# Kernel tuning notes

Hardware: AMD Instinct MI355X
Metric: run time of the kernel (lower is better)

## Reference

```python
import jax, jax.numpy as jnp
import numpy as np

B, V = 128, 128000


def setup_inputs() -> dict:
    key = jax.random.key(0)
    k1, k2, k3, k4 = jax.random.split(key, 4)
    logits = jax.random.normal(k1, (B, V), dtype=jnp.float32) * 4.0
    k = jax.random.randint(k2, (B,), 1, 1024, dtype=jnp.int32)  # top-k per row, >= 1
    p = jax.random.uniform(k3, (B,), dtype=jnp.float32, minval=0.5, maxval=1.0)
    # Exponential(1) noise, matching torch q.exponential_() in random_sample
    q = jax.random.exponential(k4, (B, V), dtype=jnp.float32)
    return {"logits": logits, "k": k, "p": p, "q": q}


def _apply_top_k_top_p(logits, k, p):
    # Faithful port of apply_top_k_top_p_pytorch (sort-ascending path).
    b, v = logits.shape
    idx = jnp.argsort(logits, axis=-1)                       # ascending, [B, V]
    ls = jnp.take_along_axis(logits, idx, axis=-1)           # sorted logits
    # top-k: threshold = (v-k)-th smallest sorted logit; values below -> -inf
    kth = jnp.take_along_axis(ls, (v - k.astype(jnp.int32))[:, None], axis=-1)  # [B, 1]
    ls = jnp.where(ls < kth, -jnp.inf, ls)
    # top-p: mask smallest tail whose cumulative prob <= 1 - p (never mask last col)
    probs_sort = jax.nn.softmax(ls, axis=-1)
    csum = jnp.cumsum(probs_sort, axis=-1)
    top_p_mask = csum <= (1.0 - p)[:, None]
    top_p_mask = top_p_mask.at[:, -1].set(False)
    ls = jnp.where(top_p_mask, -jnp.inf, ls)
    # scatter back to original vocab order
    rows = jnp.arange(b)[:, None]
    return jnp.zeros_like(logits).at[rows, idx].set(ls)


def reference(logits, k, p, q):
    # forward_native with logprobs_mode='raw_logprobs' (returns sampled ids)
    masked = _apply_top_k_top_p(logits, k, p)
    probs = jax.nn.softmax(masked, axis=-1)                  # fp32 softmax
    # Gumbel-max / exponential-race sampling: argmax(probs / Exp(1))
    token_ids = jnp.argmax(probs / q, axis=-1)
    return token_ids
```

## Files before the change

### kernel.cpp

```cpp
#include <hip/hip_runtime.h>
#include <stdint.h>

#define V 128000
#define NROWS 128
#define NSG 25
#define SG_ELEMS (V / NSG)
#define NF4 (SG_ELEMS / 4)
#define UNR 5
#define SCAP 256
#define CAPK (NSG * SCAP)
#define SELK 2048
#define ZCAP 1024
#define NBINS 4096
#define THRESH 8.0f

typedef unsigned long long ull;

__device__ __forceinline__ uint32_t f2key(uint32_t b) {
    return (b & 0x80000000u) ? ~b : (b | 0x80000000u);
}
__device__ __forceinline__ float key2f(uint32_t u) {
    uint32_t b = (u & 0x80000000u) ? (u & 0x7FFFFFFFu) : ~u;
    return __uint_as_float(b);
}

__global__ __launch_bounds__(256) void k_gather(const float* __restrict__ logits,
                                                const float* __restrict__ q,
                                                uint32_t* __restrict__ scnt,
                                                ull* __restrict__ list,
                                                uint32_t* __restrict__ zcnt,
                                                ull* __restrict__ zlist) {
    __shared__ ull lbuf[SCAP];
    __shared__ uint32_t lcnt;
    const int row = blockIdx.x / NSG;
    const int slice = blockIdx.x % NSG;
    const int t = threadIdx.x;
    if (t == 0) lcnt = 0;
    __syncthreads();

    const float4* lb = (const float4*)(logits + (size_t)row * V + (size_t)slice * SG_ELEMS);
    const float4* qb = (const float4*)(q + (size_t)row * V + (size_t)slice * SG_ELEMS);

    float4 lv[UNR], qv[UNR];
#pragma unroll
    for (int u = 0; u < UNR; ++u) lv[u] = lb[t + 256 * u];
#pragma unroll
    for (int u = 0; u < UNR; ++u) qv[u] = qb[t + 256 * u];

#pragma unroll
    for (int u = 0; u < UNR; ++u) {
        const int bidx = slice * SG_ELEMS + (t + 256 * u) * 4;
        const float4 v = lv[u];
        if (v.x >= THRESH) { unsigned p = atomicAdd(&lcnt, 1u); if (p < SCAP) lbuf[p] = ((ull)f2key(__float_as_uint(v.x)) << 32) | (unsigned)(bidx + 0); }
        if (v.y >= THRESH) { unsigned p = atomicAdd(&lcnt, 1u); if (p < SCAP) lbuf[p] = ((ull)f2key(__float_as_uint(v.y)) << 32) | (unsigned)(bidx + 1); }
        if (v.z >= THRESH) { unsigned p = atomicAdd(&lcnt, 1u); if (p < SCAP) lbuf[p] = ((ull)f2key(__float_as_uint(v.z)) << 32) | (unsigned)(bidx + 2); }
        if (v.w >= THRESH) { unsigned p = atomicAdd(&lcnt, 1u); if (p < SCAP) lbuf[p] = ((ull)f2key(__float_as_uint(v.w)) << 32) | (unsigned)(bidx + 3); }
        const float4 w = qv[u];
        if (w.x == 0.f) { unsigned p0 = atomicAdd(zcnt, 1u); if (p0 < ZCAP) zlist[p0] = ((ull)row << 32) | (unsigned)(bidx + 0); }
        if (w.y == 0.f) { unsigned p0 = atomicAdd(zcnt, 1u); if (p0 < ZCAP) zlist[p0] = ((ull)row << 32) | (unsigned)(bidx + 1); }
        if (w.z == 0.f) { unsigned p0 = atomicAdd(zcnt, 1u); if (p0 < ZCAP) zlist[p0] = ((ull)row << 32) | (unsigned)(bidx + 2); }
        if (w.w == 0.f) { unsigned p0 = atomicAdd(zcnt, 1u); if (p0 < ZCAP) zlist[p0] = ((ull)row << 32) | (unsigned)(bidx + 3); }
    }
    __syncthreads();
    uint32_t c = min(lcnt, (uint32_t)SCAP);
    ull* seg = list + (size_t)(row * NSG + slice) * SCAP;
    for (int i = t; i < (int)c; i += 256) seg[i] = lbuf[i];
    if (t == 0) scnt[row * NSG + slice] = c;
}

__global__ __launch_bounds__(1024) void k_final(const ull* __restrict__ list,
                                                const uint32_t* __restrict__ scnt,
                                                const int* __restrict__ kk,
                                                const float* __restrict__ pp,
                                                const float* __restrict__ q,
                                                const float* __restrict__ logits,
                                                const ull* __restrict__ zlist,
                                                const uint32_t* __restrict__ zcnt,
                                                int* __restrict__ out) {
    __shared__ ull cand[CAPK];
    __shared__ ull skeys[SELK];
    __shared__ uint32_t hist[NBINS];
    __shared__ uint32_t binoff[NBINS];
    __shared__ uint32_t wsumH[16];
    __shared__ int soff[NSG + 1];
    __shared__ float wtot[16], woff[16];
    __shared__ float wr[16];
    __shared__ int wi[16];
    __shared__ float sZ1, sZ2;
    __shared__ int snkeep, sJ;
    __shared__ uint32_t sKmin, sKmax, sB, sNsel, sCnt2, sB0;

    const int row = blockIdx.x;
    const int t = threadIdx.x;
    const int lane = t & 63;
    const int wave = t >> 6;

    if (t == 0) {
        int acc = 0;
        for (int s2 = 0; s2 < NSG; ++s2) {
            soff[s2] = acc;
            acc += (int)min(scnt[row * NSG + s2], (uint32_t)SCAP);
        }
        soff[NSG] = acc;
    }
    __syncthreads();
    int n_c = soff[NSG];
    const int krow0 = max(kk[row], 1);

    for (int s2 = 0; s2 < NSG; ++s2) {
        const int c0 = soff[s2], c1 = soff[s2 + 1];
        const ull* seg = list + (size_t)(row * NSG + s2) * SCAP;
        for (int i = c0 + t; i < c1; i += 1024) cand[i] = seg[i - c0];
    }
    __syncthreads();

    if (n_c < krow0) {
        for (int i = t; i < NBINS; i += 1024) hist[i] = 0;
        if (t == 0) sCnt2 = 0;
        __syncthreads();
        const float* lr = logits + (size_t)row * V;
        for (int i = t; i < V; i += 1024)
            atomicAdd(&hist[f2key(__float_as_uint(lr[i])) >> 20], 1u);
        __syncthreads();
        if (t == 0) {
            uint32_t acc = 0; int bin = NBINS - 1;
            for (; bin > 0; --bin) { acc += hist[bin]; if (acc >= (uint32_t)krow0) break; }
            sB0 = (uint32_t)bin;
        }
        __syncthreads();
        const uint32_t b0 = sB0;
        for (int i = t; i < V; i += 1024) {
            uint32_t u = f2key(__float_as_uint(lr[i]));
            if ((u >> 20) >= b0) {
                unsigned p = atomicAdd(&sCnt2, 1u);
                if (p < CAPK) cand[p] = ((ull)u << 32) | (unsigned)i;
            }
        }
        __syncthreads();
        n_c = (int)min(sCnt2, (uint32_t)CAPK);
    }
    if (n_c <= 0) { if (t == 0) out[row] = 0; return; }
    const int krow = min(krow0, n_c);

    if (t == 0) { sKmin = 0xFFFFFFFFu; sKmax = 0; }
    for (int i = t; i < NBINS; i += 1024) hist[i] = 0;
    __syncthreads();
    uint32_t lmin = 0xFFFFFFFFu, lmax = 0;
    for (int i = t; i < n_c; i += 1024) {
        uint32_t v = (uint32_t)(cand[i] >> 32);
        lmin = min(lmin, v); lmax = max(lmax, v);
    }
    atomicMin(&sKmin, lmin); atomicMax(&sKmax, lmax);
    __syncthreads();
    const uint32_t kmin = sKmin;
    const float scale = 4095.0f / fmaxf((float)(sKmax - kmin), 1.0f);
    for (int i = t; i < n_c; i += 1024) {
        uint32_t v = (uint32_t)(cand[i] >> 32);
        int bn = min((int)((float)(v - kmin) * scale), NBINS - 1);
        atomicAdd(&hist[bn], 1u);
    }
    __syncthreads();
    const uint32_t h0 = hist[4 * t], h1 = hist[4 * t + 1],
                   h2 = hist[4 * t + 2], h3 = hist[4 * t + 3];
    const uint32_t ct = h0 + h1 + h2 + h3;
    int ssum = (int)ct;
#pragma unroll
    for (int d = 1; d < 64; d <<= 1) {
        int o = __shfl_down(ssum, d);
        if (lane + d < 64) ssum += o;
    }
    if (lane == 0) wsumH[wave] = (uint32_t)ssum;
    __syncthreads();
    if (t == 0) {
        uint32_t acc = 0;
        for (int w = 15; w >= 0; --w) { uint32_t tmp = wsumH[w]; wsumH[w] = acc; acc += tmp; }
    }
    __syncthreads();
    const uint32_t Hincl = (uint32_t)ssum + wsumH[wave];
    const uint32_t Hexcl = Hincl - ct;
    if (Hexcl < (uint32_t)krow && (uint32_t)krow <= Hincl) {
        uint32_t hh[4] = { h0, h1, h2, h3 };
        uint32_t acc = Hexcl;
        for (int j = 3; j >= 0; --j) {
            if (acc + hh[j] >= (uint32_t)krow) {
                sB = (uint32_t)(4 * t + j);
                sNsel = min(acc + hh[j], (uint32_t)SELK);
                break;
            }
            acc += hh[j];
        }
    }
    {
        const uint32_t g3 = Hexcl;
        const uint32_t g2 = g3 + h3;
        const uint32_t g1 = g2 + h2;
        const uint32_t g0 = g1 + h1;
        hist[4 * t] = g0;  hist[4 * t + 1] = g1;
        hist[4 * t + 2] = g2;  hist[4 * t + 3] = g3;
        binoff[4 * t] = g0;  binoff[4 * t + 1] = g1;
        binoff[4 * t + 2] = g2;  binoff[4 * t + 3] = g3;
    }
    __syncthreads();
    const uint32_t b = sB;
    for (int i = t; i < n_c; i += 1024) {
        ull key = cand[i];
        uint32_t v = (uint32_t)(key >> 32);
        int bn = min((int)((float)(v - kmin) * scale), NBINS - 1);
        if ((uint32_t)bn >= b) {
            unsigned pos = atomicAdd(&hist[bn], 1u);
            if (pos < SELK) skeys[pos] = key;
        }
    }
    __syncthreads();
    const int nsel = (int)sNsel;
#pragma unroll
    for (int j = 0; j < 4; ++j) {
        const int bn = 4 * t + j;
        if ((uint32_t)bn < b) continue;
        const int s0 = (int)binoff[bn];
        if (s0 >= SELK) continue;
        const int e0 = (int)min(hist[bn], (uint32_t)SELK);
        for (int a = s0 + 1; a < e0; ++a) {
            ull kv = skeys[a];
            int bp = a - 1;
            while (bp >= s0 && skeys[bp] < kv) { skeys[bp + 1] = skeys[bp]; --bp; }
            skeys[bp + 1] = kv;
        }
    }
    __syncthreads();

    const uint32_t Tkey = (uint32_t)(skeys[krow - 1] >> 32);
    if (t == 0) {
        int lo = krow, hi = nsel;
        while (lo < hi) {
            int mid = (lo + hi) >> 1;
            if ((uint32_t)(skeys[mid] >> 32) >= Tkey) lo = mid + 1; else hi = mid;
        }
        snkeep = lo;
        sJ = 0;
    }
    __syncthreads();
    const int n_keep = snkeep;
    const float m = key2f((uint32_t)(skeys[0] >> 32));

    float le[4], lp[4];
    float run = 0.f;
    const int ibase = t * 4;
#pragma unroll
    for (int j2 = 0; j2 < 4; ++j2) {
        int i = ibase + j2;
        float val = 0.f;
        if (i < n_keep) val = expf(key2f((uint32_t)(skeys[i] >> 32)) - m);
        le[j2] = val;
        lp[j2] = run; run += val;
    }
    float incl = run;
#pragma unroll
    for (int d = 1; d < 64; d <<= 1) {
        float o = __shfl_up(incl, d);
        if (lane >= d) incl += o;
    }
    if (lane == 63) wtot[wave] = incl;
    __syncthreads();
    if (t == 0) {
        float acc = 0.f;
        for (int w = 0; w < 16; ++w) { woff[w] = acc; acc += wtot[w]; }
        sZ1 = acc;
    }
    __syncthreads();
    const float Z1 = sZ1;
    const float thr = pp[row] * Z1;
    const float texcl = woff[wave] + (incl - run);
    int c = 0;
#pragma unroll
    for (int j2 = 0; j2 < 4; ++j2) {
        int i = ibase + j2;
        if (i < n_keep && (texcl + lp[j2]) < thr) c++;
    }
#pragma unroll
    for (int d = 1; d < 64; d <<= 1) c += __shfl_xor(c, d);
    if (lane == 0) atomicAdd(&sJ, c);
    __syncthreads();
    const int J = sJ;
    if (t == 0) sZ2 = Z1;
    __syncthreads();
    if (J < n_keep) {
#pragma unroll
        for (int j2 = 0; j2 < 4; ++j2) {
            int i = ibase + j2;
            if (i == J) sZ2 = texcl + lp[j2];
        }
    }
    __syncthreads();
    const float Z2 = sZ2;

    float br = -1.f; int bi = 0x7fffffff;
#pragma unroll
    for (int j2 = 0; j2 < 4; ++j2) {
        int i = ibase + j2;
        if (i < J) {
            int idx = (int)(skeys[i] & 0xffffffffu);
            float qv = q[(size_t)row * V + idx];
            float r = (le[j2] / Z2) / qv;
            if (r > br || (r == br && idx < bi)) { br = r; bi = idx; }
        }
    }
#pragma unroll
    for (int d = 1; d < 64; d <<= 1) {
        float orr = __shfl_xor(br, d);
        int oi = __shfl_xor(bi, d);
        if (orr > br || (orr == br && oi < bi)) { br = orr; bi = oi; }
    }
    if (lane == 0) { wr[wave] = br; wi[wave] = bi; }
    __syncthreads();
    if (t == 0) {
        float bb = wr[0]; int bbi = wi[0];
        for (int w = 1; w < 16; ++w) {
            if (wr[w] > bb || (wr[w] == bb && wi[w] < bbi)) { bb = wr[w]; bbi = wi[w]; }
        }
        int nanidx = 0x7fffffff;
        int nz = (int)min(*zcnt, (uint32_t)ZCAP);
        ull lastkept = skeys[J - 1];
        for (int e = 0; e < nz; ++e) {
            ull ent = zlist[e];
            if ((int)(ent >> 32) != row) continue;
            int zi = (int)(ent & 0xffffffffu);
            uint32_t kb = f2key(__float_as_uint(logits[(size_t)row * V + zi]));
            ull key64 = ((ull)kb << 32) | (unsigned)zi;
            if (key64 < lastkept) nanidx = min(nanidx, zi);
        }
        out[row] = (nanidx != 0x7fffffff) ? nanidx : bbi;
    }
}

extern "C" void kernel_launch(void* const* d_in, const int* in_sizes, int n_in,
                              void* d_out, int out_size, void* d_ws, size_t ws_size,
                              hipStream_t stream) {
    const float* logits = (const float*)d_in[0];
    const int* kk       = (const int*)d_in[1];
    const float* pp     = (const float*)d_in[2];
    const float* q      = (const float*)d_in[3];
    int* out            = (int*)d_out;

    char* ws = (char*)d_ws;
    uint32_t* zcnt = (uint32_t*)ws;
    uint32_t* scnt = (uint32_t*)(ws + 1024);
    ull* zlist = (ull*)(ws + 16384);
    ull* list  = (ull*)(ws + 32768);

    hipMemsetAsync(d_ws, 0, 1024, stream);

    hipLaunchKernelGGL(k_gather, dim3(NROWS * NSG), dim3(256),  0, stream,
                       logits, q, scnt, list, zcnt, zlist);
    hipLaunchKernelGGL(k_final,  dim3(NROWS),       dim3(1024), 0, stream,
                       list, scnt, kk, pp, q, logits, zlist, zcnt, out);
}
```

Baseline: 60.58 us.

## Process two rows per gather block and parallelize candidate compaction in final kernel

The gather kernel now has each block handle the same slice for two rows, halving the grid to 1600 blocks and doubling per-thread work. In the final kernel, the serial prefix sum over slice counts becomes a wave shuffle scan. The per-slice copy loop is flattened into one parallel loop over all slice slots. The aim is to cut block scheduling overhead and serial latency in the final kernel, at the cost of less memory-level parallelism per block in the gather stage.

```diff
diff --git a/kernel.cpp b/kernel.cpp
--- a/kernel.cpp
+++ b/kernel.cpp
@@ -5,7 +5,6 @@
 #define NROWS 128
 #define NSG 25
 #define SG_ELEMS (V / NSG)
-#define NF4 (SG_ELEMS / 4)
 #define UNR 5
 #define SCAP 256
 #define CAPK (NSG * SCAP)
@@ -13,6 +12,8 @@
 #define ZCAP 1024
 #define NBINS 4096
 #define THRESH 8.0f
+#define NPAIR (NROWS / 2)
+#define NBLK (NPAIR * NSG)
 
 typedef unsigned long long ull;
 
@@ -30,42 +31,51 @@
                                                 ull* __restrict__ list,
                                                 uint32_t* __restrict__ zcnt,
                                                 ull* __restrict__ zlist) {
-    __shared__ ull lbuf[SCAP];
-    __shared__ uint32_t lcnt;
-    const int row = blockIdx.x / NSG;
+    __shared__ ull lbufA[SCAP], lbufB[SCAP];
+    __shared__ uint32_t lcntA, lcntB;
+    const int pair = blockIdx.x / NSG;
     const int slice = blockIdx.x % NSG;
+    const int rowA = pair * 2, rowB = pair * 2 + 1;
     const int t = threadIdx.x;
-    if (t == 0) lcnt = 0;
-    __syncthreads();
-
-    const float4* lb = (const float4*)(logits + (size_t)row * V + (size_t)slice * SG_ELEMS);
-    const float4* qb = (const float4*)(q + (size_t)row * V + (size_t)slice * SG_ELEMS);
-
-    float4 lv[UNR], qv[UNR];
-#pragma unroll
-    for (int u = 0; u < UNR; ++u) lv[u] = lb[t + 256 * u];
-#pragma unroll
-    for (int u = 0; u < UNR; ++u) qv[u] = qb[t + 256 * u];
-
-#pragma unroll
-    for (int u = 0; u < UNR; ++u) {
-        const int bidx = slice * SG_ELEMS + (t + 256 * u) * 4;
-        const float4 v = lv[u];
-        if (v.x >= THRESH) { unsigned p = atomicAdd(&lcnt, 1u); if (p < SCAP) lbuf[p] = ((ull)f2key(__float_as_uint(v.x)) << 32) | (unsigned)(bidx + 0); }
-        if (v.y >= THRESH) { unsigned p = atomicAdd(&lcnt, 1u); if (p < SCAP) lbuf[p] = ((ull)f2key(__float_as_uint(v.y)) << 32) | (unsigned)(bidx + 1); }
-        if (v.z >= THRESH) { unsigned p = atomicAdd(&lcnt, 1u); if (p < SCAP) lbuf[p] = ((ull)f2key(__float_as_uint(v.z)) << 32) | (unsigned)(bidx + 2); }
-        if (v.w >= THRESH) { unsigned p = atomicAdd(&lcnt, 1u); if (p < SCAP) lbuf[p] = ((ull)f2key(__float_as_uint(v.w)) << 32) | (unsigned)(bidx + 3); }
-        const float4 w = qv[u];
-        if (w.x == 0.f) { unsigned p0 = atomicAdd(zcnt, 1u); if (p0 < ZCAP) zlist[p0] = ((ull)row << 32) | (unsigned)(bidx + 0); }
-        if (w.y == 0.f) { unsigned p0 = atomicAdd(zcnt, 1u); if (p0 < ZCAP) zlist[p0] = ((ull)row << 32) | (unsigned)(bidx + 1); }
-        if (w.z == 0.f) { unsigned p0 = atomicAdd(zcnt, 1u); if (p0 < ZCAP) zlist[p0] = ((ull)row << 32) | (unsigned)(bidx + 2); }
-        if (w.w == 0.f) { unsigned p0 = atomicAdd(zcnt, 1u); if (p0 < ZCAP) zlist[p0] = ((ull)row << 32) | (unsigned)(bidx + 3); }
-    }
-    __syncthreads();
-    uint32_t c = min(lcnt, (uint32_t)SCAP);
-    ull* seg = list + (size_t)(row * NSG + slice) * SCAP;
-    for (int i = t; i < (int)c; i += 256) seg[i] = lbuf[i];
-    if (t == 0) scnt[row * NSG + slice] = c;
+    if (t == 0) { lcntA = 0; lcntB = 0; }
+    __syncthreads();
+
+#define DO_ROW(row, lbuf, lcnt)                                                                    \
+    {                                                                                              \
+        const float4* lb = (const float4*)(logits + (size_t)(row) * V + (size_t)slice * SG_ELEMS); \
+        const float4* qb = (const float4*)(q + (size_t)(row) * V + (size_t)slice * SG_ELEMS);      \
+        float4 lv[UNR], qv[UNR];                                                                   \
+        _Pragma("unroll")                                                                          \
+        for (int u = 0; u < UNR; ++u) lv[u] = lb[t + 256 * u];                                     \
+        _Pragma("unroll")                                                                          \
+        for (int u = 0; u < UNR; ++u) qv[u] = qb[t + 256 * u];                                     \
+        _Pragma("unroll")                                                                          \
+        for (int u = 0; u < UNR; ++u) {                                                            \
+            const int bidx = slice * SG_ELEMS + (t + 256 * u) * 4;                                 \
+            const float4 v = lv[u];                                                                \
+            if (v.x >= THRESH) { unsigned p = atomicAdd(&lcnt, 1u); if (p < SCAP) lbuf[p] = ((ull)f2key(__float_as_uint(v.x)) << 32) | (unsigned)(bidx + 0); } \
+            if (v.y >= THRESH) { unsigned p = atomicAdd(&lcnt, 1u); if (p < SCAP) lbuf[p] = ((ull)f2key(__float_as_uint(v.y)) << 32) | (unsigned)(bidx + 1); } \
+            if (v.z >= THRESH) { unsigned p = atomicAdd(&lcnt, 1u); if (p < SCAP) lbuf[p] = ((ull)f2key(__float_as_uint(v.z)) << 32) | (unsigned)(bidx + 2); } \
+            if (v.w >= THRESH) { unsigned p = atomicAdd(&lcnt, 1u); if (p < SCAP) lbuf[p] = ((ull)f2key(__float_as_uint(v.w)) << 32) | (unsigned)(bidx + 3); } \
+            const float4 w = qv[u];                                                                \
+            if (w.x == 0.f) { unsigned p0 = atomicAdd(zcnt, 1u); if (p0 < ZCAP) zlist[p0] = ((ull)(row) << 32) | (unsigned)(bidx + 0); } \
+            if (w.y == 0.f) { unsigned p0 = atomicAdd(zcnt, 1u); if (p0 < ZCAP) zlist[p0] = ((ull)(row) << 32) | (unsigned)(bidx + 1); } \
+            if (w.z == 0.f) { unsigned p0 = atomicAdd(zcnt, 1u); if (p0 < ZCAP) zlist[p0] = ((ull)(row) << 32) | (unsigned)(bidx + 2); } \
+            if (w.w == 0.f) { unsigned p0 = atomicAdd(zcnt, 1u); if (p0 < ZCAP) zlist[p0] = ((ull)(row) << 32) | (unsigned)(bidx + 3); } \
+        }                                                                                          \
+    }
+
+    DO_ROW(rowA, lbufA, lcntA)
+    DO_ROW(rowB, lbufB, lcntB)
+#undef DO_ROW
+    __syncthreads();
+    const uint32_t cA = min(lcntA, (uint32_t)SCAP);
+    const uint32_t cB = min(lcntB, (uint32_t)SCAP);
+    ull* segA = list + (size_t)(rowA * NSG + slice) * SCAP;
+    ull* segB = list + (size_t)(rowB * NSG + slice) * SCAP;
+    for (int i = t; i < (int)cA; i += 256) segA[i] = lbufA[i];
+    for (int i = t; i < (int)cB; i += 256) segB[i] = lbufB[i];
+    if (t == 0) { scnt[rowA * NSG + slice] = cA; scnt[rowB * NSG + slice] = cB; }
 }
 
 __global__ __launch_bounds__(1024) void k_final(const ull* __restrict__ list,
@@ -95,22 +105,27 @@
     const int lane = t & 63;
     const int wave = t >> 6;
 
-    if (t == 0) {
-        int acc = 0;
-        for (int s2 = 0; s2 < NSG; ++s2) {
-            soff[s2] = acc;
-            acc += (int)min(scnt[row * NSG + s2], (uint32_t)SCAP);
-        }
-        soff[NSG] = acc;
+    if (t < 64) {
+        uint32_t c = (lane < NSG) ? min(scnt[row * NSG + lane], (uint32_t)SCAP) : 0u;
+        uint32_t x = c;
+#pragma unroll
+        for (int d = 1; d < 32; d <<= 1) {
+            uint32_t o = __shfl_up(x, d);
+            if (lane >= d) x += o;
+        }
+        if (lane == 0) soff[0] = 0;
+        if (lane < NSG) soff[lane + 1] = (int)x;
     }
     __syncthreads();
     int n_c = soff[NSG];
     const int krow0 = max(kk[row], 1);
 
-    for (int s2 = 0; s2 < NSG; ++s2) {
+    for (int i = t; i < NSG * SCAP; i += 1024) {
+        const int s2 = i >> 8;
+        const int idx = i & (SCAP - 1);
         const int c0 = soff[s2], c1 = soff[s2 + 1];
-        const ull* seg = list + (size_t)(row * NSG + s2) * SCAP;
-        for (int i = c0 + t; i < c1; i += 1024) cand[i] = seg[i - c0];
+        if (idx < c1 - c0)
+            cand[c0 + idx] = list[(size_t)(row * NSG + s2) * SCAP + idx];
     }
     __syncthreads();
 
@@ -350,8 +365,8 @@
 
     hipMemsetAsync(d_ws, 0, 1024, stream);
 
-    hipLaunchKernelGGL(k_gather, dim3(NROWS * NSG), dim3(256),  0, stream,
+    hipLaunchKernelGGL(k_gather, dim3(NBLK),  dim3(256),  0, stream,
                        logits, q, scnt, list, zcnt, zlist);
-    hipLaunchKernelGGL(k_final,  dim3(NROWS),       dim3(1024), 0, stream,
+    hipLaunchKernelGGL(k_final,  dim3(NROWS), dim3(1024), 0, stream,
                        list, scnt, kk, pp, q, logits, zlist, zcnt, out);
 }
```

New measurement: 57.61 us. -4.9%, faster.

## Use fewer larger gather slices, parallel prefix of segment counts, flat candidate copy

Applied to the files above, without the earlier changes.

Splits each row into 16 slices instead of 25, so the gather kernel uses a strided loop in place of a fully unrolled five-load prefetch, and per-slice capacity rises to 512. In the final kernel, the serial single-thread prefix sum over slice counts becomes a wave shuffle scan, and the per-segment copy loop becomes one flat loop over all slots. The aim is to cut serial work in the final kernel's setup and lower launch block count, at the cost of less memory-level parallelism in the gather (fewer blocks, no upfront loads).

```diff
diff --git a/kernel.cpp b/kernel.cpp
--- a/kernel.cpp
+++ b/kernel.cpp
@@ -3,11 +3,10 @@
 
 #define V 128000
 #define NROWS 128
-#define NSG 25
+#define NSG 16
 #define SG_ELEMS (V / NSG)
-#define NF4 (SG_ELEMS / 4)
-#define UNR 5
-#define SCAP 256
+#define NQ4 (SG_ELEMS / 4)
+#define SCAP 512
 #define CAPK (NSG * SCAP)
 #define SELK 2048
 #define ZCAP 1024
@@ -41,28 +40,21 @@
     const float4* lb = (const float4*)(logits + (size_t)row * V + (size_t)slice * SG_ELEMS);
     const float4* qb = (const float4*)(q + (size_t)row * V + (size_t)slice * SG_ELEMS);
 
-    float4 lv[UNR], qv[UNR];
-#pragma unroll
-    for (int u = 0; u < UNR; ++u) lv[u] = lb[t + 256 * u];
-#pragma unroll
-    for (int u = 0; u < UNR; ++u) qv[u] = qb[t + 256 * u];
-
-#pragma unroll
-    for (int u = 0; u < UNR; ++u) {
-        const int bidx = slice * SG_ELEMS + (t + 256 * u) * 4;
-        const float4 v = lv[u];
+    for (int i = t; i < NQ4; i += 256) {
+        const float4 v = lb[i];
+        const float4 w = qb[i];
+        const int bidx = slice * SG_ELEMS + i * 4;
         if (v.x >= THRESH) { unsigned p = atomicAdd(&lcnt, 1u); if (p < SCAP) lbuf[p] = ((ull)f2key(__float_as_uint(v.x)) << 32) | (unsigned)(bidx + 0); }
         if (v.y >= THRESH) { unsigned p = atomicAdd(&lcnt, 1u); if (p < SCAP) lbuf[p] = ((ull)f2key(__float_as_uint(v.y)) << 32) | (unsigned)(bidx + 1); }
         if (v.z >= THRESH) { unsigned p = atomicAdd(&lcnt, 1u); if (p < SCAP) lbuf[p] = ((ull)f2key(__float_as_uint(v.z)) << 32) | (unsigned)(bidx + 2); }
         if (v.w >= THRESH) { unsigned p = atomicAdd(&lcnt, 1u); if (p < SCAP) lbuf[p] = ((ull)f2key(__float_as_uint(v.w)) << 32) | (unsigned)(bidx + 3); }
-        const float4 w = qv[u];
         if (w.x == 0.f) { unsigned p0 = atomicAdd(zcnt, 1u); if (p0 < ZCAP) zlist[p0] = ((ull)row << 32) | (unsigned)(bidx + 0); }
         if (w.y == 0.f) { unsigned p0 = atomicAdd(zcnt, 1u); if (p0 < ZCAP) zlist[p0] = ((ull)row << 32) | (unsigned)(bidx + 1); }
         if (w.z == 0.f) { unsigned p0 = atomicAdd(zcnt, 1u); if (p0 < ZCAP) zlist[p0] = ((ull)row << 32) | (unsigned)(bidx + 2); }
         if (w.w == 0.f) { unsigned p0 = atomicAdd(zcnt, 1u); if (p0 < ZCAP) zlist[p0] = ((ull)row << 32) | (unsigned)(bidx + 3); }
     }
     __syncthreads();
-    uint32_t c = min(lcnt, (uint32_t)SCAP);
+    const uint32_t c = min(lcnt, (uint32_t)SCAP);
     ull* seg = list + (size_t)(row * NSG + slice) * SCAP;
     for (int i = t; i < (int)c; i += 256) seg[i] = lbuf[i];
     if (t == 0) scnt[row * NSG + slice] = c;
@@ -95,22 +87,27 @@
     const int lane = t & 63;
     const int wave = t >> 6;
 
-    if (t == 0) {
-        int acc = 0;
-        for (int s2 = 0; s2 < NSG; ++s2) {
-            soff[s2] = acc;
-            acc += (int)min(scnt[row * NSG + s2], (uint32_t)SCAP);
-        }
-        soff[NSG] = acc;
+    if (t < 64) {
+        uint32_t c = (lane < NSG) ? min(scnt[row * NSG + lane], (uint32_t)SCAP) : 0u;
+        uint32_t x = c;
+#pragma unroll
+        for (int d = 1; d < 32; d <<= 1) {
+            uint32_t o = __shfl_up(x, d);
+            if (lane >= d) x += o;
+        }
+        if (lane == 0) soff[0] = 0;
+        if (lane < NSG) soff[lane + 1] = (int)x;
     }
     __syncthreads();
     int n_c = soff[NSG];
     const int krow0 = max(kk[row], 1);
 
-    for (int s2 = 0; s2 < NSG; ++s2) {
+    for (int i = t; i < NSG * SCAP; i += 1024) {
+        const int s2 = i >> 9;
+        const int idx = i & (SCAP - 1);
         const int c0 = soff[s2], c1 = soff[s2 + 1];
-        const ull* seg = list + (size_t)(row * NSG + s2) * SCAP;
-        for (int i = c0 + t; i < c1; i += 1024) cand[i] = seg[i - c0];
+        if (idx < c1 - c0)
+            cand[c0 + idx] = list[(size_t)(row * NSG + s2) * SCAP + idx];
     }
     __syncthreads();
 
```

New measurement: 55.22 us. 8.9% less time.
